# Optimization experiments

Measured on AMD Instinct MI355X. Metric: run time of the kernel, lower is better.

The kernel has to match this reference:

```python
import jax, jax.numpy as jnp
import numpy as np

B, N, F_IN = 8, 1024, 128
H, F_OUT = 4, 64
NEG_INF = -9e15


def setup_inputs() -> dict:
    key = jax.random.key(0)
    k1, k2, k3, k4 = jax.random.split(key, 4)
    x = jax.random.normal(k1, (B, N, F_IN), dtype=jnp.float32)
    adj = jax.random.randint(k2, (B, N, N), 0, 2, dtype=jnp.int32)
    W = jax.random.normal(k3, (F_IN, H * F_OUT), dtype=jnp.float32) * 0.05
    a = jax.random.normal(k4, (H, 2 * F_OUT), dtype=jnp.float32)
    return {"x": x, "adj": adj, "W": W, "a": a}


def reference(x, adj, W, a):
    # x: [B,N,F_in], adj: [B,N,N], W: [F_in, H*F_out], a: [H, 2*F_out]
    Bs, Ns, _ = x.shape
    Hh = a.shape[0]
    Fo = a.shape[1] // 2
    h = (x @ W).reshape(Bs, Ns, Hh, Fo)            # [B,N,H,F]
    # e_{bnmh} = a . cat(h_i, h_j) = a_src . h_n + a_dst . h_m  (no O(N^2) concat)
    a_src, a_dst = a[:, :Fo], a[:, Fo:]
    e_src = jnp.einsum('bnhf,hf->bnh', h, a_src)    # [B,N,H]
    e_dst = jnp.einsum('bmhf,hf->bmh', h, a_dst)    # [B,N,H]
    e = e_src[:, :, None, :] + e_dst[:, None, :, :]  # [B,N,N,H]
    e = jax.nn.leaky_relu(e, negative_slope=0.2)
    e = jnp.where(adj[..., None] > 0, e, NEG_INF)
    attention = jax.nn.softmax(e, axis=2)           # softmax over neighbors m
    h_prime = jnp.einsum('bnmh,bmhf->bnhf', attention, h)
    return h_prime.mean(axis=2)                     # [B,N,F_out]
```

## Files before the change

### kernel.cpp

```cpp
#include <hip/hip_runtime.h>
#include <math.h>

#define Bsz 8
#define Nsz 1024
#define FIN 128
#define Hh  4
#define FO  64
#define COLS 256
#define TN  16
#define TM  32
#define NT  (Nsz/TM)
#define BN  (Bsz*Nsz)
#define XSTR 136
#define LOG2E  1.44269504088896340f
#define CSHIFT 17.3123404906675611f
#define NEG08C (-0.8f * CSHIFT)

typedef __attribute__((ext_vector_type(8))) short short8;
typedef __attribute__((ext_vector_type(4))) float f32x4;

static __device__ inline ushort f2bf(float f) {
    uint u = __float_as_uint(f);
    u += 0x7FFFu + ((u >> 16) & 1u);
    return (ushort)(u >> 16);
}

static __device__ inline float fexp2(float x) {
#if __has_builtin(__builtin_amdgcn_exp2f)
    return __builtin_amdgcn_exp2f(x);
#else
    float r; asm("v_exp_f32 %0, %1" : "=v"(r) : "v"(x));
    return r;
#endif
}

__global__ __launch_bounds__(256) void gat_prep(const float* __restrict__ W,
                                                ushort* __restrict__ Wt,
                                                const int* __restrict__ adj,
                                                uint* __restrict__ ab)
{
    if (blockIdx.x < 1024) {
        const long g = (long)blockIdx.x * 256 + threadIdx.x;
        const int4* src = (const int4*)(adj + g * 32);
        uint m = 0u;
        #pragma unroll
        for (int i = 0; i < 8; i++) {
            int4 v = src[i];
            m |= (v.x > 0 ? 1u : 0u) << (i*4);
            m |= (v.y > 0 ? 1u : 0u) << (i*4 + 1);
            m |= (v.z > 0 ? 1u : 0u) << (i*4 + 2);
            m |= (v.w > 0 ? 1u : 0u) << (i*4 + 3);
        }
        ab[g] = m;
    } else {
        const int g = (blockIdx.x - 1024) * 256 + threadIdx.x;
        const int n = g >> 3, kc = (g & 7) * 16;
        ushort u[16];
        #pragma unroll
        for (int i = 0; i < 16; i++) u[i] = f2bf(W[(kc + i) * COLS + n]);
        int4* dst = (int4*)(Wt + n * FIN + kc);
        dst[0] = ((int4*)u)[0];
        dst[1] = ((int4*)u)[1];
    }
}

__global__ __launch_bounds__(256) void gat_proj(
    const float* __restrict__ x, const ushort* __restrict__ Wt,
    const float* __restrict__ a, ushort* __restrict__ h_gB,
    float* __restrict__ es_g, float* __restrict__ ed_g)
{
    __shared__ ushort xs[16 * XSTR];
    const int j    = threadIdx.x;
    const int w    = j >> 6, lane = j & 63, quad = lane >> 4, n16 = lane & 15;
    const int b    = blockIdx.x >> 6, mt16 = blockIdx.x & 63;
    const long rowbase = (long)b * Nsz + mt16 * 16;

    short8 bfr[4][4];
    #pragma unroll
    for (int kk = 0; kk < 4; kk++)
        #pragma unroll
        for (int c4 = 0; c4 < 4; c4++)
            bfr[kk][c4] = *(const short8*)(Wt + (w*64 + c4*16 + n16) * FIN + kk*32 + quad*8);

    {
        const int r = j >> 4, k0 = (j & 15) * 8;
        const float4* g4 = (const float4*)(x + (rowbase + r) * FIN + k0);
        float4 v0 = g4[0], v1 = g4[1];
        ushort u[8] = { f2bf(v0.x), f2bf(v0.y), f2bf(v0.z), f2bf(v0.w),
                        f2bf(v1.x), f2bf(v1.y), f2bf(v1.z), f2bf(v1.w) };
        *(int4*)(xs + r * XSTR + k0) = *(int4*)u;
    }
    __syncthreads();

    f32x4 acc[4];
    #pragma unroll
    for (int c4 = 0; c4 < 4; c4++)
        #pragma unroll
        for (int r = 0; r < 4; r++) acc[c4][r] = 0.f;

    #pragma unroll
    for (int kk = 0; kk < 4; kk++) {
        short8 af = *(const short8*)(xs + n16 * XSTR + kk*32 + quad*8);
        #pragma unroll
        for (int c4 = 0; c4 < 4; c4++)
            acc[c4] = __builtin_amdgcn_mfma_f32_16x16x32_bf16(af, bfr[kk][c4], acc[c4], 0, 0, 0);
    }

    const int mtile = mt16 >> 1;
    const int kbase = (mt16 & 1) * 16 + quad * 4;
    #pragma unroll
    for (int c4 = 0; c4 < 4; c4++) {
        uint2 pk;
        pk.x = (uint)f2bf(acc[c4][0]) | ((uint)f2bf(acc[c4][1]) << 16);
        pk.y = (uint)f2bf(acc[c4][2]) | ((uint)f2bf(acc[c4][3]) << 16);
        const int c = w*64 + c4*16 + n16;
        *(uint2*)(h_gB + (((long)(b*32 + mtile) * COLS + c) * 32 + kbase)) = pk;
    }

    float aS[4], aD[4];
    #pragma unroll
    for (int c4 = 0; c4 < 4; c4++) {
        aS[c4] = a[w * (2*FO) + c4*16 + n16];
        aD[c4] = a[w * (2*FO) + FO + c4*16 + n16];
    }
    #pragma unroll
    for (int reg = 0; reg < 4; reg++) {
        float ps = 0.f, pd = 0.f;
        #pragma unroll
        for (int c4 = 0; c4 < 4; c4++) {
            ps = fmaf(acc[c4][reg], aS[c4], ps);
            pd = fmaf(acc[c4][reg], aD[c4], pd);
        }
        #pragma unroll
        for (int off = 1; off < 16; off <<= 1) {
            ps += __shfl_xor(ps, off, 64);
            pd += __shfl_xor(pd, off, 64);
        }
        if (n16 == 0) {
            const long row = rowbase + quad*4 + reg;
            es_g[(long)w * BN + row] = ps * LOG2E - CSHIFT;
            ed_g[(long)w * BN + row] = pd * LOG2E;
        }
    }
}

__global__ __launch_bounds__(256, 2) void gat_attn(
    const uint* __restrict__ ab, const ushort* __restrict__ h_gB,
    const float* __restrict__ es_g, const float* __restrict__ ed_g,
    float* __restrict__ out)
{
    __shared__ __align__(16) char smem[Hh * TN * 65 * 4];
    __shared__ uint abT[TN][36];
    float (*edT)[Nsz]      = (float (*)[Nsz])smem;
    float (*o_lds)[TN][65] = (float (*)[TN][65])smem;

    const int j    = threadIdx.x;
    const int w    = j >> 6, lane = j & 63, quad = lane >> 4, n16 = lane & 15;
    const int b    = blockIdx.x, n0 = blockIdx.y * TN;
    const long rowb = (long)b * Nsz + n0;

    {
        const float* src = ed_g + (long)w * BN + (long)b * Nsz + lane * 16;
        float* dst = &edT[w][lane * 16];
        #pragma unroll
        for (int i = 0; i < 4; i++)
            *(float4*)(dst + i*4) = *(const float4*)(src + i*4);
    }
    if (j < 128) {
        const int r = j >> 3, c = (j & 7) * 4;
        *(int4*)&abT[r][c] = *(const int4*)(ab + (rowb + r) * 32 + c);
    }
    const float esC = es_g[(long)w * BN + rowb + n16];
    __syncthreads();

    f32x4 acc[4], accl;
    #pragma unroll
    for (int c4 = 0; c4 < 4; c4++)
        #pragma unroll
        for (int r = 0; r < 4; r++) acc[c4][r] = 0.f;
    #pragma unroll
    for (int r = 0; r < 4; r++) accl[r] = 0.f;

    short8 ones;
    #pragma unroll
    for (int i = 0; i < 8; i++) ones[i] = (short)0x3F80;

    const ushort* hb = h_gB + (long)b * (Nsz * COLS);
    short8 h0[4], h1[4];

#define PRE_H(t, H) {                                                           \
    const ushort* hp = hb + (long)(t) * (COLS * TM);                            \
    _Pragma("unroll")                                                           \
    for (int c4 = 0; c4 < 4; c4++)                                              \
        H[c4] = *(const short8*)(hp + (w*64 + c4*16 + n16) * TM + quad*8); }

#define SUBT(t, HC, ABU) {                                                      \
    f32x4 ev0 = *(const f32x4*)&edT[w][(t)*32 + quad*8];                        \
    f32x4 ev1 = *(const f32x4*)&edT[w][(t)*32 + quad*8 + 4];                    \
    const uint b8 = ((ABU) >> (quad*8)) & 0xffu;                                \
    uint pk[4];                                                                 \
    _Pragma("unroll")                                                           \
    for (int p2 = 0; p2 < 4; p2++) {                                            \
        float t0 = esC + (p2 < 2 ? ev0[p2*2]     : ev1[(p2-2)*2]);              \
        float t1 = esC + (p2 < 2 ? ev0[p2*2 + 1] : ev1[(p2-2)*2 + 1]);          \
        float u0 = fmaxf(t0, fmaf(0.2f, t0, NEG08C));                           \
        float u1 = fmaxf(t1, fmaf(0.2f, t1, NEG08C));                           \
        float e0 = fexp2(u0), e1 = fexp2(u1);                                   \
        e0 = (b8 & (1u << (p2*2)))     ? e0 : 0.f;                              \
        e1 = (b8 & (1u << (p2*2 + 1))) ? e1 : 0.f;                              \
        asm("v_cvt_pk_bf16_f32 %0, %1, %2" : "=v"(pk[p2]) : "v"(e0), "v"(e1));  \
    }                                                                           \
    short8 af;                                                                  \
    ((uint*)&af)[0] = pk[0]; ((uint*)&af)[1] = pk[1];                           \
    ((uint*)&af)[2] = pk[2]; ((uint*)&af)[3] = pk[3];                           \
    accl = __builtin_amdgcn_mfma_f32_16x16x32_bf16(af, ones, accl, 0, 0, 0);    \
    _Pragma("unroll")                                                           \
    for (int c4 = 0; c4 < 4; c4++)                                              \
        acc[c4] = __builtin_amdgcn_mfma_f32_16x16x32_bf16(af, HC[c4], acc[c4], 0, 0, 0); }

    PRE_H(0, h0);
    uint4 abq = *(const uint4*)&abT[n16][0];
    for (int t4 = 0; t4 < NT; t4 += 4) {
        const int tn = (t4 + 4 < NT) ? t4 + 4 : 0;
        uint4 abn = *(const uint4*)&abT[n16][tn];
        PRE_H(t4 + 1, h1);  SUBT(t4,     h0, abq.x);
        PRE_H(t4 + 2, h0);  SUBT(t4 + 1, h1, abq.y);
        PRE_H(t4 + 3, h1);  SUBT(t4 + 2, h0, abq.z);
        if (t4 + 4 < NT) PRE_H(t4 + 4, h0);
        SUBT(t4 + 3, h1, abq.w);
        abq = abn;
    }

    float rinv[4];
    #pragma unroll
    for (int reg = 0; reg < 4; reg++) rinv[reg] = 0.25f / accl[reg];

    __syncthreads();
    #pragma unroll
    for (int c4 = 0; c4 < 4; c4++)
        #pragma unroll
        for (int reg = 0; reg < 4; reg++)
            o_lds[w][quad*4 + reg][c4*16 + n16] = acc[c4][reg] * rinv[reg];
    __syncthreads();

    {
        const int f = j & 63, rb4 = j >> 6;
        #pragma unroll
        for (int i = 0; i < 4; i++) {
            const int r = i*4 + rb4;
            const float s = o_lds[0][r][f] + o_lds[1][r][f]
                          + o_lds[2][r][f] + o_lds[3][r][f];
            out[(rowb + r) * FO + f] = s;
        }
    }
#undef PRE_H
#undef SUBT
}

extern "C" void kernel_launch(void* const* d_in, const int* in_sizes, int n_in,
                              void* d_out, int out_size, void* d_ws, size_t ws_size,
                              hipStream_t stream) {
    const float* x   = (const float*)d_in[0];
    const int*   adj = (const int*)d_in[1];
    const float* W   = (const float*)d_in[2];
    const float* a   = (const float*)d_in[3];
    float* out = (float*)d_out;

    ushort* Wt   = (ushort*)d_ws;
    ushort* h_gB = Wt + (size_t)COLS * FIN;
    float*  es_g = (float*)(h_gB + (size_t)BN * COLS);
    float*  ed_g = es_g + (size_t)Hh * BN;
    uint*   abb  = (uint*)(ed_g + (size_t)Hh * BN);

    gat_prep<<<dim3(1032),          dim3(256), 0, stream>>>(W, Wt, adj, abb);
    gat_proj<<<dim3(Bsz*Nsz/16),    dim3(256), 0, stream>>>(x, Wt, a, h_gB, es_g, ed_g);
    gat_attn<<<dim3(Bsz, Nsz/TN),   dim3(256), 0, stream>>>(abb, h_gB, es_g, ed_g, out);
}
```

Before: 109.6 us.

## Fold prep kernel into proj and attn, split attention neighbors across two warp groups

Removes the separate prep kernel. Each proj block now converts W to bf16 into LDS itself, and the attention kernel reads raw int32 adj and packs it into bitmasks using ballot. The attention block grows to 512 threads, and two groups of four waves each handle half of the neighbor tiles. Their partial accumulators are combined through LDS before normalization. This trades a launch and an intermediate buffer for redundant W conversion in every proj block (512 blocks, each with about 68KB of LDS) and for reading int32 adj directly in attention.

```diff
diff --git a/kernel.cpp b/kernel.cpp
--- a/kernel.cpp
+++ b/kernel.cpp
@@ -34,53 +34,17 @@
 #endif
 }
 
-__global__ __launch_bounds__(256) void gat_prep(const float* __restrict__ W,
-                                                ushort* __restrict__ Wt,
-                                                const int* __restrict__ adj,
-                                                uint* __restrict__ ab)
-{
-    if (blockIdx.x < 1024) {
-        const long g = (long)blockIdx.x * 256 + threadIdx.x;
-        const int4* src = (const int4*)(adj + g * 32);
-        uint m = 0u;
-        #pragma unroll
-        for (int i = 0; i < 8; i++) {
-            int4 v = src[i];
-            m |= (v.x > 0 ? 1u : 0u) << (i*4);
-            m |= (v.y > 0 ? 1u : 0u) << (i*4 + 1);
-            m |= (v.z > 0 ? 1u : 0u) << (i*4 + 2);
-            m |= (v.w > 0 ? 1u : 0u) << (i*4 + 3);
-        }
-        ab[g] = m;
-    } else {
-        const int g = (blockIdx.x - 1024) * 256 + threadIdx.x;
-        const int n = g >> 3, kc = (g & 7) * 16;
-        ushort u[16];
-        #pragma unroll
-        for (int i = 0; i < 16; i++) u[i] = f2bf(W[(kc + i) * COLS + n]);
-        int4* dst = (int4*)(Wt + n * FIN + kc);
-        dst[0] = ((int4*)u)[0];
-        dst[1] = ((int4*)u)[1];
-    }
-}
-
 __global__ __launch_bounds__(256) void gat_proj(
-    const float* __restrict__ x, const ushort* __restrict__ Wt,
+    const float* __restrict__ x, const float* __restrict__ W,
     const float* __restrict__ a, ushort* __restrict__ h_gB,
     float* __restrict__ es_g, float* __restrict__ ed_g)
 {
     __shared__ ushort xs[16 * XSTR];
+    __shared__ ushort wLDS[COLS * XSTR];
     const int j    = threadIdx.x;
     const int w    = j >> 6, lane = j & 63, quad = lane >> 4, n16 = lane & 15;
     const int b    = blockIdx.x >> 6, mt16 = blockIdx.x & 63;
     const long rowbase = (long)b * Nsz + mt16 * 16;
-
-    short8 bfr[4][4];
-    #pragma unroll
-    for (int kk = 0; kk < 4; kk++)
-        #pragma unroll
-        for (int c4 = 0; c4 < 4; c4++)
-            bfr[kk][c4] = *(const short8*)(Wt + (w*64 + c4*16 + n16) * FIN + kk*32 + quad*8);
 
     {
         const int r = j >> 4, k0 = (j & 15) * 8;
@@ -90,7 +54,26 @@
                         f2bf(v1.x), f2bf(v1.y), f2bf(v1.z), f2bf(v1.w) };
         *(int4*)(xs + r * XSTR + k0) = *(int4*)u;
     }
-    __syncthreads();
+
+    #pragma unroll
+    for (int i8 = 0; i8 < 16; i8++) {
+        float wv[8];
+        #pragma unroll
+        for (int ii = 0; ii < 8; ii++) wv[ii] = W[(i8*8 + ii) * COLS + j];
+        uint pk4[4];
+        #pragma unroll
+        for (int i2 = 0; i2 < 4; i2++)
+            asm("v_cvt_pk_bf16_f32 %0, %1, %2" : "=v"(pk4[i2]) : "v"(wv[2*i2]), "v"(wv[2*i2+1]));
+        *(int4*)(wLDS + j * XSTR + i8*8) = *(int4*)pk4;
+    }
+    __syncthreads();
+
+    short8 bfr[4][4];
+    #pragma unroll
+    for (int kk = 0; kk < 4; kk++)
+        #pragma unroll
+        for (int c4 = 0; c4 < 4; c4++)
+            bfr[kk][c4] = *(const short8*)(wLDS + (w*64 + c4*16 + n16) * XSTR + kk*32 + quad*8);
 
     f32x4 acc[4];
     #pragma unroll
@@ -144,31 +127,41 @@
     }
 }
 
-__global__ __launch_bounds__(256, 2) void gat_attn(
-    const uint* __restrict__ ab, const ushort* __restrict__ h_gB,
+__global__ __launch_bounds__(512, 4) void gat_attn(
+    const int* __restrict__ adj, const ushort* __restrict__ h_gB,
     const float* __restrict__ es_g, const float* __restrict__ ed_g,
     float* __restrict__ out)
 {
-    __shared__ __align__(16) char smem[Hh * TN * 65 * 4];
-    __shared__ uint abT[TN][36];
+    __shared__ __align__(16) char smem[20*1024 + Hh * TN * 65 * 4];
     float (*edT)[Nsz]      = (float (*)[Nsz])smem;
-    float (*o_lds)[TN][65] = (float (*)[TN][65])smem;
+    uint  (*abT)[36]       = (uint (*)[36])(smem + 16*1024);
+    float (*o_lds)[TN][65] = (float (*)[TN][65])(smem + 20*1024);
 
     const int j    = threadIdx.x;
-    const int w    = j >> 6, lane = j & 63, quad = lane >> 4, n16 = lane & 15;
+    const int g    = j >> 8;
+    const int jg   = j & 255;
+    const int w    = jg >> 6, lane = jg & 63, quad = lane >> 4, n16 = lane & 15;
     const int b    = blockIdx.x, n0 = blockIdx.y * TN;
     const long rowb = (long)b * Nsz + n0;
 
     {
-        const float* src = ed_g + (long)w * BN + (long)b * Nsz + lane * 16;
-        float* dst = &edT[w][lane * 16];
-        #pragma unroll
-        for (int i = 0; i < 4; i++)
-            *(float4*)(dst + i*4) = *(const float4*)(src + i*4);
-    }
-    if (j < 128) {
-        const int r = j >> 3, c = (j & 7) * 4;
-        *(int4*)&abT[r][c] = *(const int4*)(ab + (rowb + r) * 32 + c);
+        const float* src = ed_g + (long)w * BN + (long)b * Nsz + g*512 + lane*8;
+        float* dst = &edT[w][g*512 + lane*8];
+        *(float4*)dst       = *(const float4*)src;
+        *(float4*)(dst + 4) = *(const float4*)(src + 4);
+    }
+    {
+        const int* ap = adj + rowb * (long)Nsz;
+        #pragma unroll 4
+        for (int k = 0; k < 32; k++) {
+            const int idx = k*512 + j;
+            const int v = ap[idx];
+            const unsigned long long m = __ballot(v > 0);
+            if (lane == 0) {
+                const int row = idx >> 10, col0 = idx & 1023;
+                *(uint2*)&abT[row][col0 >> 5] = make_uint2((uint)m, (uint)(m >> 32));
+            }
+        }
     }
     const float esC = es_g[(long)w * BN + rowb + n16];
     __syncthreads();
@@ -218,36 +211,50 @@
     for (int c4 = 0; c4 < 4; c4++)                                              \
         acc[c4] = __builtin_amdgcn_mfma_f32_16x16x32_bf16(af, HC[c4], acc[c4], 0, 0, 0); }
 
-    PRE_H(0, h0);
-    uint4 abq = *(const uint4*)&abT[n16][0];
-    for (int t4 = 0; t4 < NT; t4 += 4) {
-        const int tn = (t4 + 4 < NT) ? t4 + 4 : 0;
+    PRE_H(g*16, h0);
+    uint4 abq = *(const uint4*)&abT[n16][g*16];
+    for (int t4i = 0; t4i < 16; t4i += 4) {
+        const int t4 = g*16 + t4i;
+        const int tn = (t4i + 4 < 16) ? (t4 + 4) : g*16;
         uint4 abn = *(const uint4*)&abT[n16][tn];
         PRE_H(t4 + 1, h1);  SUBT(t4,     h0, abq.x);
         PRE_H(t4 + 2, h0);  SUBT(t4 + 1, h1, abq.y);
         PRE_H(t4 + 3, h1);  SUBT(t4 + 2, h0, abq.z);
-        if (t4 + 4 < NT) PRE_H(t4 + 4, h0);
+        if (t4i + 4 < 16) PRE_H(t4 + 4, h0);
         SUBT(t4 + 3, h1, abq.w);
         abq = abn;
     }
 
-    float rinv[4];
-    #pragma unroll
-    for (int reg = 0; reg < 4; reg++) rinv[reg] = 0.25f / accl[reg];
-
-    __syncthreads();
-    #pragma unroll
-    for (int c4 = 0; c4 < 4; c4++)
-        #pragma unroll
-        for (int reg = 0; reg < 4; reg++)
-            o_lds[w][quad*4 + reg][c4*16 + n16] = acc[c4][reg] * rinv[reg];
-    __syncthreads();
-
-    {
-        const int f = j & 63, rb4 = j >> 6;
-        #pragma unroll
-        for (int i = 0; i < 4; i++) {
-            const int r = i*4 + rb4;
+    __syncthreads();
+    float* mg = (float*)smem;
+    if (g == 1) {
+        #pragma unroll
+        for (int c4 = 0; c4 < 4; c4++)
+            #pragma unroll
+            for (int r = 0; r < 4; r++) mg[(c4*4 + r) * 256 + jg] = acc[c4][r];
+        #pragma unroll
+        for (int r = 0; r < 4; r++) mg[(16 + r) * 256 + jg] = accl[r];
+    }
+    __syncthreads();
+    if (g == 0) {
+        float rinv[4];
+        #pragma unroll
+        for (int r = 0; r < 4; r++)
+            rinv[r] = 0.25f / (accl[r] + mg[(16 + r) * 256 + jg]);
+        #pragma unroll
+        for (int c4 = 0; c4 < 4; c4++)
+            #pragma unroll
+            for (int r = 0; r < 4; r++)
+                o_lds[w][quad*4 + r][c4*16 + n16] =
+                    (acc[c4][r] + mg[(c4*4 + r) * 256 + jg]) * rinv[r];
+    }
+    __syncthreads();
+
+    {
+        const int f = j & 63, r2 = (j >> 6) & 7;
+        #pragma unroll
+        for (int i = 0; i < 2; i++) {
+            const int r = i*8 + r2;
             const float s = o_lds[0][r][f] + o_lds[1][r][f]
                           + o_lds[2][r][f] + o_lds[3][r][f];
             out[(rowb + r) * FO + f] = s;
@@ -266,13 +273,10 @@
     const float* a   = (const float*)d_in[3];
     float* out = (float*)d_out;
 
-    ushort* Wt   = (ushort*)d_ws;
-    ushort* h_gB = Wt + (size_t)COLS * FIN;
+    ushort* h_gB = (ushort*)d_ws;
     float*  es_g = (float*)(h_gB + (size_t)BN * COLS);
     float*  ed_g = es_g + (size_t)Hh * BN;
-    uint*   abb  = (uint*)(ed_g + (size_t)Hh * BN);
-
-    gat_prep<<<dim3(1032),          dim3(256), 0, stream>>>(W, Wt, adj, abb);
-    gat_proj<<<dim3(Bsz*Nsz/16),    dim3(256), 0, stream>>>(x, Wt, a, h_gB, es_g, ed_g);
-    gat_attn<<<dim3(Bsz, Nsz/TN),   dim3(256), 0, stream>>>(abb, h_gB, es_g, ed_g, out);
-}
+
+    gat_proj<<<dim3(Bsz*Nsz/16),  dim3(256), 0, stream>>>(x, W, a, h_gB, es_g, ed_g);
+    gat_attn<<<dim3(Bsz, Nsz/TN), dim3(512), 0, stream>>>(adj, h_gB, es_g, ed_g, out);
+}
```

Measured after the change: 109.2 us (median of 2 runs). About the same (-0.4%).
